# Kernel tuning notes

Measured on AMD Instinct MI355X. Metric: run time of the kernel, lower is better.

Reference implementation:

```python
import jax, jax.numpy as jnp
import numpy as np

B, N, FIN, FOUT = 64, 784, 64, 64
EPS = 1e-5
NEG = -1e9  # masked-logit fill (avoids -inf NaNs on isolated nodes)


def setup_inputs() -> dict:
    key = jax.random.key(0)
    ks = jax.random.split(key, 6)
    init = lambda k, shape, fan: (jax.random.normal(k, shape, jnp.float32) / np.float32(np.sqrt(fan)))
    return {
        "node_features": jax.random.normal(ks[0], (B, N, FIN), jnp.float32),
        "adjacency_matrix": jax.random.randint(ks[1], (N, N), 0, 2, jnp.int32),
        "W_self": init(ks[2], (FOUT, FIN), FIN),
        "b_self": jnp.zeros((FOUT,), jnp.float32),
        "W_nb": init(ks[3], (FOUT, FIN), FIN),
        "b_nb": jnp.zeros((FOUT,), jnp.float32),
        "a_src": init(ks[4], (FIN,), 2 * FIN),   # attention weight half acting on x_i
        "a_dst": init(ks[5], (FIN,), 2 * FIN),   # attention weight half acting on x_j
        "b_att": jnp.zeros((), jnp.float32),
        "ln_gamma": jnp.ones((FOUT,), jnp.float32),
        "ln_beta": jnp.zeros((FOUT,), jnp.float32),
    }


def reference(node_features, adjacency_matrix, W_self, b_self, W_nb, b_nb,
              a_src, a_dst, b_att, ln_gamma, ln_beta):
    # mask[i, j] = node j is a neighbor of node i
    mask = adjacency_matrix != 0  # [N, N]

    self_feats = node_features @ W_self.T + b_self      # [B, N, Fout]
    nb_proj = node_features @ W_nb.T + b_nb              # [B, N, Fout]

    # attention(cat[x_i, x_j]) == x_i @ a_src + x_j @ a_dst + b_att
    src = node_features @ a_src                          # [B, N]
    dst = node_features @ a_dst                          # [B, N]
    logits = src[:, :, None] + dst[:, None, :] + b_att   # [B, N, N]
    logits = jnp.where(mask[None], logits, NEG)
    # softmax over neighbors j; zero out non-edges (handles isolated nodes -> 0)
    w = jax.nn.softmax(logits, axis=2) * mask[None]
    agg = jnp.einsum('bij,bjf->bif', w, nb_proj)         # [B, N, Fout]

    combined = self_feats + agg                           # dropout: eval mode (identity)
    mu = combined.mean(-1, keepdims=True)
    var = combined.var(-1, keepdims=True)
    normed = (combined - mu) * jax.lax.rsqrt(var + EPS) * ln_gamma + ln_beta
    return jax.nn.relu(normed)
```

## Files before the change

kernel.cpp:

```cpp
#include <hip/hip_runtime.h>


typedef unsigned short u16;
typedef unsigned int u32;
typedef short bf16x8 __attribute__((ext_vector_type(8)));
typedef float f32x4 __attribute__((ext_vector_type(4)));

#define NNODE 784
#define MP 832
#define BUFU 13312

__device__ __forceinline__ float b2f(u16 h) {
  union { u32 u; float f; } v; v.u = ((u32)h) << 16; return v.f;
}
__device__ __forceinline__ u16 f2b(float f) {
  union { float f; u32 u; } v; v.f = f;
  u32 r = (v.u + 0x7FFFu + ((v.u >> 16) & 1u)) >> 16;
  return (u16)r;
}
__device__ __forceinline__ void gload16(const u16* g, u16* l) {
  __builtin_amdgcn_global_load_lds((const __attribute__((address_space(1))) u32*)g,
                                   (__attribute__((address_space(3))) u32*)l, 16, 0, 0);
}

__global__ __launch_bounds__(256) void k_prep(const int* __restrict__ adj,
                                              const float* __restrict__ Ws,
                                              const float* __restrict__ Wn,
                                              u16* __restrict__ A,
                                              u16* __restrict__ W2) {
  int t = threadIdx.x;
  if (blockIdx.x < 364) {
    int idx8 = blockIdx.x * 256 + t;
    int i = idx8 / 104, j8 = idx8 - i * 104;
    __align__(16) u16 o[8];
    if (i < NNODE && j8 < 98) {
      const int4* ap = (const int4*)(adj + (size_t)i * NNODE + j8 * 8);
      int4 a0 = ap[0], a1 = ap[1];
      o[0] = a0.x ? 0x3F80 : 0; o[1] = a0.y ? 0x3F80 : 0;
      o[2] = a0.z ? 0x3F80 : 0; o[3] = a0.w ? 0x3F80 : 0;
      o[4] = a1.x ? 0x3F80 : 0; o[5] = a1.y ? 0x3F80 : 0;
      o[6] = a1.z ? 0x3F80 : 0; o[7] = a1.w ? 0x3F80 : 0;
    } else {
#pragma unroll
      for (int q = 0; q < 8; ++q) o[q] = 0;
    }
    *(uint4*)(A + (size_t)i * MP + j8 * 8) = *(const uint4*)o;
  } else {
    int f = t >> 2, cq = t & 3;
#pragma unroll
    for (int q = 0; q < 4; ++q) {
      int c = cq * 4 + q;
      int cs = c ^ (f & 7);
      const float* src = (cs < 8) ? (Ws + f * 64 + cs * 8) : (Wn + f * 64 + (cs - 8) * 8);
      float4 v0 = ((const float4*)src)[0], v1 = ((const float4*)src)[1];
      __align__(16) u16 ob[8];
      ob[0] = f2b(v0.x); ob[1] = f2b(v0.y); ob[2] = f2b(v0.z); ob[3] = f2b(v0.w);
      ob[4] = f2b(v1.x); ob[5] = f2b(v1.y); ob[6] = f2b(v1.z); ob[7] = f2b(v1.w);
      *(uint4*)(W2 + f * 128 + c * 8) = *(const uint4*)ob;
    }
  }
}

__global__ __launch_bounds__(256) void k_b1t(const float* __restrict__ X,
                                             const float* __restrict__ adst,
                                             u16* __restrict__ Bt) {
  __shared__ float Xs[64][68];
  __shared__ float ad[64];
  __shared__ float es[64];
  int bid = blockIdx.x;
  int b = bid / 13, jt = bid - b * 13;
  int j0 = jt * 64;
  int t = threadIdx.x;
  if (b == 64) {
    int row = 4160 + (t >> 2), c = (t & 3) * 16;
    uint4 z; z.x = 0; z.y = 0; z.z = 0; z.w = 0;
    uint4* p = (uint4*)(Bt + (size_t)row * MP + j0 + c);
    p[0] = z; p[1] = z;
    return;
  }
  int jr = t >> 2, cg = t & 3;
  {
    int j = j0 + jr;
    float4 z4; z4.x = 0.f; z4.y = 0.f; z4.z = 0.f; z4.w = 0.f;
    float4 v0 = z4, v1 = z4, v2 = z4, v3 = z4;
    if (j < NNODE) {
      const float4* xp = (const float4*)(X + ((size_t)b * NNODE + j) * 64 + cg * 16);
      v0 = xp[0]; v1 = xp[1]; v2 = xp[2]; v3 = xp[3];
    }
    float4* d = (float4*)&Xs[jr][cg * 16];
    d[0] = v0; d[1] = v1; d[2] = v2; d[3] = v3;
  }
  if (t < 64) ad[t] = adst[t];
  __syncthreads();
  {
    float dot = 0.f;
#pragma unroll
    for (int q = 0; q < 16; ++q) dot += Xs[jr][cg * 16 + q] * ad[cg * 16 + q];
    dot += __shfl_xor(dot, 1);
    dot += __shfl_xor(dot, 2);
    if (cg == 0) es[jr] = (j0 + jr < NNODE) ? __expf(dot) : 0.f;
  }
  __syncthreads();
  {
    int f = t >> 2, jc = (t & 3) * 16;
    __align__(16) u16 ob[16];
#pragma unroll
    for (int q = 0; q < 16; ++q) ob[q] = f2b(es[jc + q] * Xs[jc + q][f]);
    u16* op = Bt + ((size_t)b * 64 + f) * MP + j0 + jc;
    *(uint4*)op = *(const uint4*)ob;
    *(uint4*)(op + 8) = *(const uint4*)(ob + 8);
  }
  if (t < 64) Bt[(size_t)(4096 + b) * MP + j0 + t] = f2b(es[t]);
}

__global__ __launch_bounds__(512) void k_gt(const u16* __restrict__ A,
                                            const u16* __restrict__ Bt,
                                            const u16* __restrict__ W2g,
                                            const float* __restrict__ X,
                                            const float* __restrict__ bs,
                                            const float* __restrict__ bn,
                                            const float* __restrict__ gam,
                                            const float* __restrict__ bet,
                                            float* __restrict__ out) {
  __shared__ __align__(16) u16 lds[2 * BUFU];
  __shared__ float denL[64][2];
  __shared__ float bsL[64], bnL[64], gamL[64], betL[64];
  const int t = threadIdx.x;
  const int l = t & 63, w = t >> 6;
  const int g = l >> 4, l15 = l & 15;
  const int wr = w >> 2, wc = w & 3;

  int wg = (blockIdx.x & 7) * 52 + (blockIdx.x >> 3);
  const int bp = wg / 13;
  const int it = wg - bp * 13;
  const int i0 = it * 64;
  const int nb0 = bp * 128;
  const int nd0 = 4096 + 2 * bp;

  if (t < 64) { bsL[t] = bs[t]; bnL[t] = bn[t]; gamL[t] = gam[t]; betL[t] = bet[t]; }

  f32x4 acc[2][2];
#pragma unroll
  for (int mi = 0; mi < 2; ++mi)
#pragma unroll
    for (int ni = 0; ni < 2; ++ni) acc[mi][ni] = (f32x4){0.f, 0.f, 0.f, 0.f};
  f32x4 accD[2];
  accD[0] = (f32x4){0.f, 0.f, 0.f, 0.f};
  accD[1] = (f32x4){0.f, 0.f, 0.f, 0.f};

#define STAGE(kt_, buf_)                                                          \
  {                                                                               \
    int k0_ = (kt_) * 64;                                                         \
    u16* dA_ = lds + (buf_) * BUFU;                                               \
    u16* dB_ = dA_ + 4096;                                                        \
    { int r_ = t >> 3, c_ = t & 7;                                                \
      gload16(A + (size_t)(i0 + r_) * MP + k0_ + ((c_ ^ (r_ & 7)) * 8),           \
              dA_ + w * 512); }                                                   \
    _Pragma("unroll")                                                             \
    for (int h_ = 0; h_ < 2; ++h_) {                                              \
      int s_ = h_ * 512 + t; int r_ = s_ >> 3, c_ = s_ & 7;                       \
      gload16(Bt + (size_t)(nb0 + r_) * MP + k0_ + ((c_ ^ (r_ & 7)) * 8),         \
              dB_ + h_ * 4096 + w * 512); }                                       \
    if (w < 2) { int r_ = t >> 3, c_ = t & 7;                                     \
      gload16(Bt + (size_t)(nd0 + r_) * MP + k0_ + ((c_ ^ (r_ & 7)) * 8),         \
              dB_ + 8192 + w * 512); }                                            \
  }

  STAGE(0, 0);
  __syncthreads();

  for (int kt = 0; kt < 13; ++kt) {
    int buf = kt & 1;
    if (kt < 12) STAGE(kt + 1, buf ^ 1);
    const u16* As = lds + buf * BUFU;
    const u16* Bs = As + 4096;
#pragma unroll
    for (int kk = 0; kk < 2; ++kk) {
      int q = kk * 4 + g;
      bf16x8 af[2], bfr[2];
#pragma unroll
      for (int mi = 0; mi < 2; ++mi) {
        int ra = wr * 32 + mi * 16 + l15;
        af[mi] = *(const bf16x8*)(As + ra * 64 + ((q ^ (ra & 7)) * 8));
      }
#pragma unroll
      for (int ni = 0; ni < 2; ++ni) {
        int rb = wc * 32 + ni * 16 + l15;
        bfr[ni] = *(const bf16x8*)(Bs + rb * 64 + ((q ^ (rb & 7)) * 8));
      }
#pragma unroll
      for (int mi = 0; mi < 2; ++mi)
#pragma unroll
        for (int ni = 0; ni < 2; ++ni)
          acc[mi][ni] = __builtin_amdgcn_mfma_f32_16x16x32_bf16(af[mi], bfr[ni], acc[mi][ni], 0, 0, 0);
      if (wc == 3) {
        int rd = 128 + l15;
        bf16x8 bd = *(const bf16x8*)(Bs + rd * 64 + ((q ^ (rd & 7)) * 8));
        accD[0] = __builtin_amdgcn_mfma_f32_16x16x32_bf16(af[0], bd, accD[0], 0, 0, 0);
        accD[1] = __builtin_amdgcn_mfma_f32_16x16x32_bf16(af[1], bd, accD[1], 0, 0, 0);
      }
    }
    __syncthreads();
  }
#undef STAGE

  u16* AB2 = lds;
  u16* W2l = lds + 16384;
  if (wc == 3 && l15 < 2) {
#pragma unroll
    for (int mi = 0; mi < 2; ++mi)
#pragma unroll
      for (int j = 0; j < 4; ++j)
        denL[wr * 32 + mi * 16 + g * 4 + j][l15] = accD[mi][j];
  }
#pragma unroll
  for (int q2 = 0; q2 < 2; ++q2) {
    int s = q2 * 512 + t;
    int r = s >> 3, c = s & 7;
    int i = i0 + (r & 63);
    int bq = bp * 2 + (r >> 6);
    float4 v0, v1;
    v0.x = v0.y = v0.z = v0.w = 0.f; v1 = v0;
    if (i < NNODE) {
      const float4* xp = (const float4*)(X + ((size_t)bq * NNODE + i) * 64 + c * 8);
      v0 = xp[0]; v1 = xp[1];
    }
    __align__(16) u16 ob[8];
    ob[0] = f2b(v0.x); ob[1] = f2b(v0.y); ob[2] = f2b(v0.z); ob[3] = f2b(v0.w);
    ob[4] = f2b(v1.x); ob[5] = f2b(v1.y); ob[6] = f2b(v1.z); ob[7] = f2b(v1.w);
    *(uint4*)(AB2 + r * 128 + ((c ^ (r & 7)) * 8)) = *(const uint4*)ob;
  }
#pragma unroll
  for (int q2 = 0; q2 < 2; ++q2)
    gload16(W2g + q2 * 4096 + w * 512 + l * 8, W2l + q2 * 4096 + w * 512);
  __syncthreads();

#pragma unroll
  for (int mi = 0; mi < 2; ++mi)
#pragma unroll
    for (int ni = 0; ni < 2; ++ni) {
      int col = wc * 32 + ni * 16 + l15;
      int b2 = col >> 6, f = col & 63;
#pragma unroll
      for (int j = 0; j < 4; ++j) {
        int ri = wr * 32 + mi * 16 + g * 4 + j;
        float d = denL[ri][b2];
        float rd = d > 0.f ? 1.f / d : 0.f;
        int R = b2 * 64 + ri;
        AB2[R * 128 + (((8 + (f >> 3)) ^ (R & 7)) * 8) + (f & 7)] = f2b(acc[mi][ni][j] * rd);
      }
    }
  __syncthreads();

  const int b2w = w >> 2, mf = w & 3;
  f32x4 a2[4];
#pragma unroll
  for (int nf = 0; nf < 4; ++nf) a2[nf] = (f32x4){0.f, 0.f, 0.f, 0.f};
#pragma unroll
  for (int kk = 0; kk < 4; ++kk) {
    int q2 = kk * 4 + g;
    int ra = b2w * 64 + mf * 16 + l15;
    bf16x8 af = *(const bf16x8*)(AB2 + ra * 128 + ((q2 ^ (ra & 7)) * 8));
#pragma unroll
    for (int nf = 0; nf < 4; ++nf) {
      int rb = nf * 16 + l15;
      bf16x8 bfw = *(const bf16x8*)(W2l + rb * 128 + ((q2 ^ (rb & 7)) * 8));
      a2[nf] = __builtin_amdgcn_mfma_f32_16x16x32_bf16(af, bfw, a2[nf], 0, 0, 0);
    }
  }

#pragma unroll
  for (int j = 0; j < 4; ++j) {
    int ri = mf * 16 + g * 4 + j;
    float d = denL[ri][b2w];
    float bnm = d > 0.f ? 1.f : 0.f;
    float v0 = a2[0][j] + bsL[l15]      + bnm * bnL[l15];
    float v1 = a2[1][j] + bsL[l15 + 16] + bnm * bnL[l15 + 16];
    float v2 = a2[2][j] + bsL[l15 + 32] + bnm * bnL[l15 + 32];
    float v3 = a2[3][j] + bsL[l15 + 48] + bnm * bnL[l15 + 48];
    float s1 = v0 + v1 + v2 + v3;
    float s2 = v0 * v0 + v1 * v1 + v2 * v2 + v3 * v3;
    s1 += __shfl_xor(s1, 1); s2 += __shfl_xor(s2, 1);
    s1 += __shfl_xor(s1, 2); s2 += __shfl_xor(s2, 2);
    s1 += __shfl_xor(s1, 4); s2 += __shfl_xor(s2, 4);
    s1 += __shfl_xor(s1, 8); s2 += __shfl_xor(s2, 8);
    float mu = s1 * (1.f / 64.f);
    float var = fmaxf(s2 * (1.f / 64.f) - mu * mu, 0.f);
    float inv = rsqrtf(var + 1e-5f);
    int node = i0 + ri;
    if (node < NNODE) {
      float* op = out + ((size_t)(bp * 2 + b2w) * NNODE + node) * 64;
      op[l15]      = fmaxf((v0 - mu) * inv * gamL[l15]      + betL[l15],      0.f);
      op[l15 + 16] = fmaxf((v1 - mu) * inv * gamL[l15 + 16] + betL[l15 + 16], 0.f);
      op[l15 + 32] = fmaxf((v2 - mu) * inv * gamL[l15 + 32] + betL[l15 + 32], 0.f);
      op[l15 + 48] = fmaxf((v3 - mu) * inv * gamL[l15 + 48] + betL[l15 + 48], 0.f);
    }
  }
}

extern "C" void kernel_launch(void* const* d_in, const int* in_sizes, int n_in,
                              void* d_out, int out_size, void* d_ws, size_t ws_size,
                              hipStream_t stream) {
  const float* X     = (const float*)d_in[0];
  const int*   adj   = (const int*)d_in[1];
  const float* Wself = (const float*)d_in[2];
  const float* bself = (const float*)d_in[3];
  const float* Wnb   = (const float*)d_in[4];
  const float* bnb   = (const float*)d_in[5];
  const float* adst  = (const float*)d_in[7];
  const float* gam   = (const float*)d_in[9];
  const float* bet   = (const float*)d_in[10];
  float* out = (float*)d_out;
  char* ws = (char*)d_ws;

  u16* Apad = (u16*)(ws);
  u16* W2g  = (u16*)(ws + 1490944);
  u16* Bt   = (u16*)(ws + 1507328);

  k_prep<<<dim3(365), dim3(256), 0, stream>>>(adj, Wself, Wnb, Apad, W2g);
  k_b1t <<<dim3(845), dim3(256), 0, stream>>>(X, adst, Bt);
  k_gt  <<<dim3(416), dim3(512), 0, stream>>>(Apad, Bt, W2g, X, bself, bnb, gam, bet, out);
}
```

Baseline: 34.92 us.

## Merge prep kernels into one launch and split denominator MFMAs across two waves

Combines the adjacency/weight conversion kernel and the exp-weighted feature transpose kernel into a single launch, selected by block index, which removes one kernel launch and its inter-kernel gap. In the main GEMM kernel the extra denominator MFMAs, previously all done by the wc==3 waves, are now split by k-step between the wc==2 and wc==3 waves. The two partial sums are combined through LDS using an extra barrier. It also adds a min-blocks-per-CU launch bound of 4 to k_gt, which may limit register use.

```diff
diff --git a/kernel.cpp b/kernel.cpp
--- a/kernel.cpp
+++ b/kernel.cpp
@@ -23,14 +23,18 @@
                                    (__attribute__((address_space(3))) u32*)l, 16, 0, 0);
 }
 
-__global__ __launch_bounds__(256) void k_prep(const int* __restrict__ adj,
-                                              const float* __restrict__ Ws,
-                                              const float* __restrict__ Wn,
-                                              u16* __restrict__ A,
-                                              u16* __restrict__ W2) {
-  int t = threadIdx.x;
-  if (blockIdx.x < 364) {
-    int idx8 = blockIdx.x * 256 + t;
+__global__ __launch_bounds__(256) void k_pre(const int* __restrict__ adj,
+                                             const float* __restrict__ Ws,
+                                             const float* __restrict__ Wn,
+                                             const float* __restrict__ X,
+                                             const float* __restrict__ adst,
+                                             u16* __restrict__ A,
+                                             u16* __restrict__ W2,
+                                             u16* __restrict__ Bt) {
+  const int bid = blockIdx.x;
+  const int t = threadIdx.x;
+  if (bid < 364) {
+    int idx8 = bid * 256 + t;
     int i = idx8 / 104, j8 = idx8 - i * 104;
     __align__(16) u16 o[8];
     if (i < NNODE && j8 < 98) {
@@ -45,7 +49,9 @@
       for (int q = 0; q < 8; ++q) o[q] = 0;
     }
     *(uint4*)(A + (size_t)i * MP + j8 * 8) = *(const uint4*)o;
-  } else {
+    return;
+  }
+  if (bid == 364) {
     int f = t >> 2, cq = t & 3;
 #pragma unroll
     for (int q = 0; q < 4; ++q) {
@@ -58,19 +64,14 @@
       ob[4] = f2b(v1.x); ob[5] = f2b(v1.y); ob[6] = f2b(v1.z); ob[7] = f2b(v1.w);
       *(uint4*)(W2 + f * 128 + c * 8) = *(const uint4*)ob;
     }
-  }
-}
-
-__global__ __launch_bounds__(256) void k_b1t(const float* __restrict__ X,
-                                             const float* __restrict__ adst,
-                                             u16* __restrict__ Bt) {
+    return;
+  }
   __shared__ float Xs[64][68];
   __shared__ float ad[64];
   __shared__ float es[64];
-  int bid = blockIdx.x;
-  int b = bid / 13, jt = bid - b * 13;
+  int bid2 = bid - 365;
+  int b = bid2 / 13, jt = bid2 - b * 13;
   int j0 = jt * 64;
-  int t = threadIdx.x;
   if (b == 64) {
     int row = 4160 + (t >> 2), c = (t & 3) * 16;
     uint4 z; z.x = 0; z.y = 0; z.z = 0; z.w = 0;
@@ -113,15 +114,15 @@
   if (t < 64) Bt[(size_t)(4096 + b) * MP + j0 + t] = f2b(es[t]);
 }
 
-__global__ __launch_bounds__(512) void k_gt(const u16* __restrict__ A,
-                                            const u16* __restrict__ Bt,
-                                            const u16* __restrict__ W2g,
-                                            const float* __restrict__ X,
-                                            const float* __restrict__ bs,
-                                            const float* __restrict__ bn,
-                                            const float* __restrict__ gam,
-                                            const float* __restrict__ bet,
-                                            float* __restrict__ out) {
+__global__ __launch_bounds__(512, 4) void k_gt(const u16* __restrict__ A,
+                                               const u16* __restrict__ Bt,
+                                               const u16* __restrict__ W2g,
+                                               const float* __restrict__ X,
+                                               const float* __restrict__ bs,
+                                               const float* __restrict__ bn,
+                                               const float* __restrict__ gam,
+                                               const float* __restrict__ bet,
+                                               float* __restrict__ out) {
   __shared__ __align__(16) u16 lds[2 * BUFU];
   __shared__ float denL[64][2];
   __shared__ float bsL[64], bnL[64], gamL[64], betL[64];
@@ -193,7 +194,7 @@
 #pragma unroll
         for (int ni = 0; ni < 2; ++ni)
           acc[mi][ni] = __builtin_amdgcn_mfma_f32_16x16x32_bf16(af[mi], bfr[ni], acc[mi][ni], 0, 0, 0);
-      if (wc == 3) {
+      if (wc == 2 + kk) {
         int rd = 128 + l15;
         bf16x8 bd = *(const bf16x8*)(Bs + rd * 64 + ((q ^ (rd & 7)) * 8));
         accD[0] = __builtin_amdgcn_mfma_f32_16x16x32_bf16(af[0], bd, accD[0], 0, 0, 0);
@@ -206,7 +207,7 @@
 
   u16* AB2 = lds;
   u16* W2l = lds + 16384;
-  if (wc == 3 && l15 < 2) {
+  if (wc == 2 && l15 < 2) {
 #pragma unroll
     for (int mi = 0; mi < 2; ++mi)
 #pragma unroll
@@ -233,6 +234,15 @@
 #pragma unroll
   for (int q2 = 0; q2 < 2; ++q2)
     gload16(W2g + q2 * 4096 + w * 512 + l * 8, W2l + q2 * 4096 + w * 512);
+  __syncthreads();
+
+  if (wc == 3 && l15 < 2) {
+#pragma unroll
+    for (int mi = 0; mi < 2; ++mi)
+#pragma unroll
+      for (int j = 0; j < 4; ++j)
+        denL[wr * 32 + mi * 16 + g * 4 + j][l15] += accD[mi][j];
+  }
   __syncthreads();
 
 #pragma unroll
@@ -317,7 +327,6 @@
   u16* W2g  = (u16*)(ws + 1490944);
   u16* Bt   = (u16*)(ws + 1507328);
 
-  k_prep<<<dim3(365), dim3(256), 0, stream>>>(adj, Wself, Wnb, Apad, W2g);
-  k_b1t <<<dim3(845), dim3(256), 0, stream>>>(X, adst, Bt);
-  k_gt  <<<dim3(416), dim3(512), 0, stream>>>(Apad, Bt, W2g, X, bself, bnb, gam, bet, out);
-}
+  k_pre<<<dim3(1210), dim3(256), 0, stream>>>(adj, Wself, Wnb, X, adst, Apad, W2g, Bt);
+  k_gt <<<dim3(416),  dim3(512), 0, stream>>>(Apad, Bt, W2g, X, bself, bnb, gam, bet, out);
+}
```

Result: faster. 30.20 us (-13.5%).
